# Kernel optimization log

Measured on AMD Instinct MI355X. Metric: run time of the kernel, lower is better.

The kernel has to match this reference:

```python
import jax, jax.numpy as jnp
import numpy as np

N, E = 50000, 800000
IN, HID, OUT = 128, 32, 8


def setup_inputs() -> dict:
    key = jax.random.key(0)
    ks = jax.random.split(key, 20)
    f32 = jnp.float32
    def rn(k, shape, s=0.1):
        return (jax.random.normal(k, shape, dtype=f32) * s)
    return {
        'x': jax.random.normal(ks[0], (N, IN), dtype=f32),
        'edge_index': jax.random.randint(ks[1], (2, E), 0, N, dtype=jnp.int32),
        'edge_attr': jax.random.uniform(ks[2], (E, 1), dtype=f32),
        # layer 1: heads=4, out=HID, concat -> 4*HID channels
        'w1l': rn(ks[3], (IN, 4 * HID)), 'b1l': rn(ks[4], (4 * HID,)),
        'w1r': rn(ks[5], (IN, 4 * HID)), 'b1r': rn(ks[6], (4 * HID,)),
        'w1e': rn(ks[7], (1, 4 * HID)),
        'att1': rn(ks[8], (4, HID)), 'bias1': rn(ks[9], (4 * HID,)),
        # layer 2: heads=2, out=HID, mean over heads -> HID channels
        'w2l': rn(ks[10], (4 * HID, 2 * HID)), 'b2l': rn(ks[11], (2 * HID,)),
        'w2r': rn(ks[12], (4 * HID, 2 * HID)), 'b2r': rn(ks[13], (2 * HID,)),
        'w2e': rn(ks[14], (1, 2 * HID)),
        'att2': rn(ks[15], (2, HID)), 'bias2': rn(ks[16], (HID,)),
        'wc': rn(ks[17], (HID, OUT)), 'bc': rn(ks[18], (OUT,)),
    }


def _add_self_loops(edge_index, edge_attr, n):
    # PyG GATv2Conv adds self-loops; edge feature for loops = mean of edge_attr
    loop = jnp.arange(n, dtype=edge_index.dtype)
    src = jnp.concatenate([edge_index[0], loop])
    dst = jnp.concatenate([edge_index[1], loop])
    mean_attr = jnp.broadcast_to(edge_attr.mean(axis=0), (n, edge_attr.shape[1]))
    ea = jnp.concatenate([edge_attr, mean_attr], axis=0)
    return src, dst, ea


def _gatv2(x, src, dst, eattr, Wl, bl, Wr, br, We, att, bias, heads, out, concat):
    n = x.shape[0]
    xl = (x @ Wl + bl).reshape(n, heads, out)   # source transform (messages)
    xr = (x @ Wr + br).reshape(n, heads, out)   # target transform
    e = (eattr @ We).reshape(-1, heads, out)    # edge embedding
    z = jax.nn.leaky_relu(xl[src] + xr[dst] + e, negative_slope=0.2)  # [Etot,H,D]
    score = jnp.einsum('ehd,hd->eh', z, att)
    # segment softmax over incoming edges of each destination node
    smax = jax.ops.segment_max(score, dst, num_segments=n)
    ex = jnp.exp(score - smax[dst])
    denom = jax.ops.segment_sum(ex, dst, num_segments=n)
    alpha = ex / denom[dst]                     # [Etot,H]
    agg = jax.ops.segment_sum(xl[src] * alpha[..., None], dst, num_segments=n)
    o = agg.reshape(n, heads * out) if concat else agg.mean(axis=1)
    return o + bias


def reference(x, edge_index, edge_attr, w1l, b1l, w1r, b1r, w1e, att1, bias1,
              w2l, b2l, w2r, b2r, w2e, att2, bias2, wc, bc):
    src, dst, ea = _add_self_loops(edge_index, edge_attr, x.shape[0])
    h = _gatv2(x, src, dst, ea, w1l, b1l, w1r, b1r, w1e, att1, bias1, 4, HID, True)
    h = jax.nn.elu(h)
    # dropout p=0.4 is training-only; reference is eval mode (identity)
    h = _gatv2(h, src, dst, ea, w2l, b2l, w2r, b2r, w2e, att2, bias2, 2, HID, False)
    h = jax.nn.elu(h)
    return h @ wc + bc
```

## Files before the change

### kernel.cpp

```cpp
#include <hip/hip_runtime.h>
#include <hip/hip_fp16.h>
#include <math.h>

typedef _Float16 h2_t __attribute__((ext_vector_type(2)));
typedef _Float16 h4_t __attribute__((ext_vector_type(4)));
typedef _Float16 h8_t __attribute__((ext_vector_type(8)));
typedef float f4_t __attribute__((ext_vector_type(4)));
typedef float f8_t __attribute__((ext_vector_type(8)));

#define PRE_BLOCKS 512
#define SB 512
#define NBUK_PAD 800

__device__ inline h8_t load8f_to_h8(const float* p) {
    float4 a = *(const float4*)p;
    float4 b = *(const float4*)(p + 4);
    h8_t r;
    r[0] = (_Float16)a.x; r[1] = (_Float16)a.y; r[2] = (_Float16)a.z; r[3] = (_Float16)a.w;
    r[4] = (_Float16)b.x; r[5] = (_Float16)b.y; r[6] = (_Float16)b.z; r[7] = (_Float16)b.w;
    return r;
}

__device__ inline h4_t load4f_to_h4(const float* p) {
    float4 a = *(const float4*)p;
    h4_t r;
    r[0] = (_Float16)a.x; r[1] = (_Float16)a.y; r[2] = (_Float16)a.z; r[3] = (_Float16)a.w;
    return r;
}

__device__ inline float dot8h(h8_t a, h8_t b, float s) {
    s = __builtin_amdgcn_fdot2(__builtin_shufflevector(a, a, 0, 1),
                               __builtin_shufflevector(b, b, 0, 1), s, false);
    s = __builtin_amdgcn_fdot2(__builtin_shufflevector(a, a, 2, 3),
                               __builtin_shufflevector(b, b, 2, 3), s, false);
    s = __builtin_amdgcn_fdot2(__builtin_shufflevector(a, a, 4, 5),
                               __builtin_shufflevector(b, b, 4, 5), s, false);
    s = __builtin_amdgcn_fdot2(__builtin_shufflevector(a, a, 6, 7),
                               __builtin_shufflevector(b, b, 6, 7), s, false);
    return s;
}

__device__ inline float dot4h(h4_t a, h4_t b, float s) {
    s = __builtin_amdgcn_fdot2(__builtin_shufflevector(a, a, 0, 1),
                               __builtin_shufflevector(b, b, 0, 1), s, false);
    s = __builtin_amdgcn_fdot2(__builtin_shufflevector(a, a, 2, 3),
                               __builtin_shufflevector(b, b, 2, 3), s, false);
    return s;
}

__device__ inline float elu1(float v) { return v > 0.f ? v : __expf(v) - 1.f; }

struct MA {
    const float* x;
    const float* eattr;
    const int* ei;
    const float *w1l, *b1l, *w1r, *b1r, *w1e, *att1, *bias1;
    const float *w2l, *b2l, *w2r, *b2r, *w2e, *att2, *bias2;
    const float *wc, *bc;
    float* out;
    _Float16 *xh, *xl1h, *xr1h, *h1h, *xl2h, *xr2h;
    _Float16 *p1l, *p1r, *p2l, *p2r;
    int *deg, *offb;
    unsigned* parth;
    unsigned *tstart, *tot;
    unsigned* smeanq;
    unsigned long long* tmp;
    unsigned* flags;
    float* part;
    unsigned* edges;
    int N, E, NW, NBK, CE;
    float invE;
};


__device__ inline void phase_packw(const MA& a, int g) {
    const float* W;
    _Float16* P;
    int M, lg;
    if (g < 2048)      { W = a.w1l; P = a.p1l; M = 128; lg = g; }
    else if (g < 4096) { W = a.w1r; P = a.p1r; M = 128; lg = g - 2048; }
    else if (g < 5120) { W = a.w2l; P = a.p2l; M = 64;  lg = g - 4096; }
    else               { W = a.w2r; P = a.p2r; M = 64;  lg = g - 5120; }
    int ln = lg & 63;
    int s = (lg >> 6) & 3;
    int tt = lg >> 8;
    int m = ln & 15, quad = ln >> 4;
    h8_t v;
#pragma unroll
    for (int j = 0; j < 8; ++j)
        v[j] = (_Float16)W[(size_t)(s * 32 + quad * 8 + j) * M + tt * 16 + m];
    *(h8_t*)(P + (size_t)lg * 8) = v;
}

template <int NT>
__device__ inline void phase_mm_tile(const MA& a, const _Float16* X, int rt, int lane,
                                     const _Float16* Pl, const float* bl, _Float16* Yl,
                                     const _Float16* Pr, const float* br, _Float16* Yr) {
    int nrow = lane & 15, quad = lane >> 4;
    int row = rt * 16 + nrow;
    if (row >= a.N) return;
    const _Float16* xp = X + (size_t)row * 128 + quad * 8;
    h8_t bf0 = *(const h8_t*)(xp);
    h8_t bf1 = *(const h8_t*)(xp + 32);
    h8_t bf2 = *(const h8_t*)(xp + 64);
    h8_t bf3 = *(const h8_t*)(xp + 96);
#pragma unroll
    for (int w = 0; w < 2; ++w) {
        const _Float16* P = w ? Pr : Pl;
        const float* bias = w ? br : bl;
        _Float16* Y = w ? Yr : Yl;
#pragma unroll
        for (int t2 = 0; t2 < NT; ++t2) {
            f4_t acc = {0.f, 0.f, 0.f, 0.f};
            const _Float16* pb = P + (size_t)t2 * 2048 + (size_t)lane * 8;
            acc = __builtin_amdgcn_mfma_f32_16x16x32_f16(*(const h8_t*)pb, bf0, acc, 0, 0, 0);
            acc = __builtin_amdgcn_mfma_f32_16x16x32_f16(*(const h8_t*)(pb + 512), bf1, acc, 0, 0, 0);
            acc = __builtin_amdgcn_mfma_f32_16x16x32_f16(*(const h8_t*)(pb + 1024), bf2, acc, 0, 0, 0);
            acc = __builtin_amdgcn_mfma_f32_16x16x32_f16(*(const h8_t*)(pb + 1536), bf3, acc, 0, 0, 0);
            float4 bv = *(const float4*)(bias + t2 * 16 + quad * 4);
            h4_t o;
            o[0] = (_Float16)(acc[0] + bv.x);
            o[1] = (_Float16)(acc[1] + bv.y);
            o[2] = (_Float16)(acc[2] + bv.z);
            o[3] = (_Float16)(acc[3] + bv.w);
            *(h4_t*)(Y + (size_t)row * (NT * 16) + t2 * 16 + quad * 4) = o;
        }
    }
}


__global__ __launch_bounds__(256) void k_pre(MA a) {
    if (blockIdx.x >= PRE_BLOCKS) {
        int g = (blockIdx.x - PRE_BLOCKS) * 256 + threadIdx.x;
        if (g < 6144) phase_packw(a, g);
        return;
    }
    __shared__ unsigned bh[NBUK_PAD];
    __shared__ float sd[4];
    int tx = threadIdx.x;
    for (int j = tx; j < NBUK_PAD; j += 256) bh[j] = 0u;

    int t = blockIdx.x * 256 + tx;
    const int stride = PRE_BLOCKS * 256;
    for (int i = t; i < NBUK_PAD; i += stride) a.flags[i] = 0u;
    int nchunk = (a.N * 128) >> 3;
    for (int i = t; i < nchunk; i += stride) {
        h8_t v = load8f_to_h8(a.x + (size_t)i * 8);
        *(h8_t*)(a.xh + (size_t)i * 8) = v;
    }
    float s = 0.f;
    for (int i = t; i < a.E; i += stride) s += a.eattr[i];
    for (int o = 1; o < 64; o <<= 1) s += __shfl_xor(s, o, 64);
    if ((tx & 63) == 0) sd[tx >> 6] = s;
    __syncthreads();
    if (tx == 0) a.part[blockIdx.x] = sd[0] + sd[1] + sd[2] + sd[3];

    int e0 = blockIdx.x * a.CE, e1 = min(e0 + a.CE, a.E);
    for (int e = e0 + tx; e < e1; e += 256)
        atomicAdd(&bh[((unsigned)a.ei[a.E + e]) >> 6], 1u);
    __syncthreads();
    for (int j = tx; j < NBUK_PAD; j += 256)
        a.parth[(size_t)blockIdx.x * NBUK_PAD + j] = bh[j];
}


__global__ __launch_bounds__(512, 1) void k_colscan(MA a) {
    __shared__ unsigned lds[512];
    __shared__ unsigned sbase;
    __shared__ float sd[8];
    int tx = threadIdx.x;
    int b = blockIdx.x;
    unsigned v = a.parth[(size_t)tx * NBUK_PAD + b];
    lds[tx] = v;
    __syncthreads();
    for (int o = 1; o < 512; o <<= 1) {
        unsigned u = (tx >= o) ? lds[tx - o] : 0u;
        __syncthreads();
        lds[tx] += u;
        __syncthreads();
    }
    unsigned T = lds[511];
    unsigned excl = lds[tx] - v;
    if (tx == 0) {
        unsigned run = 0;
        if (b == 0) {
            atomicExch(&a.flags[0], (2u << 30) | T);
        } else {
            atomicExch(&a.flags[b], (1u << 30) | T);
            int j = b - 1;
            while (true) {
                unsigned f = atomicAdd(&a.flags[j], 0u);
                unsigned st = f >> 30;
                if (st == 0u) continue;
                run += f & 0x3FFFFFFFu;
                if (st == 2u) break;
                --j;
            }
            atomicExch(&a.flags[b], (2u << 30) | (run + T));
        }
        a.tstart[b] = run;
        a.tot[b] = T;
        sbase = run;
    }
    __syncthreads();
    a.parth[(size_t)tx * NBUK_PAD + b] = sbase + excl;

    if (b == 0) {
        float s = a.part[tx];
        for (int o = 1; o < 64; o <<= 1) s += __shfl_xor(s, o, 64);
        if ((tx & 63) == 0) sd[tx >> 6] = s;
        __syncthreads();
        if (tx == 0) {
            float m = 0.f;
#pragma unroll
            for (int k = 0; k < 8; ++k) m += sd[k];
            a.smeanq[0] = (unsigned)__float2int_rn(m * a.invE * 255.f);
        }
    }
}


__global__ __launch_bounds__(256) void k_scatter(MA a) {
    int bid = blockIdx.x;
    if (bid < a.NW) {
        int wid = bid * 4 + (threadIdx.x >> 6);
        int ntile = (a.N + 15) / 16;
        if (wid < ntile)
            phase_mm_tile<8>(a, a.xh, wid, threadIdx.x & 63,
                             a.p1l, a.b1l, a.xl1h, a.p1r, a.b1r, a.xr1h);
        return;
    }
    __shared__ unsigned cur[NBUK_PAD];
    int s = bid - a.NW;
    int tx = threadIdx.x;
    for (int j = tx; j < NBUK_PAD; j += 256)
        cur[j] = a.parth[(size_t)s * NBUK_PAD + j];
    __syncthreads();
    int e0 = s * a.CE, e1 = min(e0 + a.CE, a.E);
    for (int e = e0 + tx; e < e1; e += 256) {
        int d = a.ei[a.E + e];
        unsigned src = (unsigned)a.ei[e];
        unsigned q = (unsigned)__float2int_rn(a.eattr[e] * 255.f);
        unsigned pos = atomicAdd(&cur[d >> 6], 1u);
        a.tmp[pos] = ((unsigned long long)(unsigned)(d & 63) << 32) |
                     (unsigned long long)(src | (q << 24));
    }
}


__global__ __launch_bounds__(256) void k_fine(MA a) {
    __shared__ int hist[64];
    __shared__ unsigned cur[64];
    __shared__ unsigned sm;
    int b = blockIdx.x;
    int tx = threadIdx.x;
    int n0 = b << 6;
    int nn = min(64, a.N - n0);
    unsigned ts = a.tstart[b], T = a.tot[b];
    if (tx < 64) hist[tx] = 0;
    if (tx == 0) sm = a.smeanq[0];
    __syncthreads();
    for (unsigned i = tx; i < T; i += 256) {
        unsigned long long v = a.tmp[ts + i];
        atomicAdd(&hist[(int)((v >> 32) & 63)], 1);
    }
    __syncthreads();
    if (tx < 64) {
        int deg1 = hist[tx] + 1;
        int vsc = deg1;
#pragma unroll
        for (int o = 1; o < 64; o <<= 1) {
            int u = __shfl_up(vsc, o, 64);
            if (tx >= o) vsc += u;
        }
        int off = (int)ts + n0 + (vsc - deg1);
        if (tx < nn) {
            a.offb[n0 + tx] = off;
            a.deg[n0 + tx] = deg1;
            a.edges[off] = (unsigned)(n0 + tx) | (sm << 24);
        }
        cur[tx] = (unsigned)(off + 1);
    }
    __syncthreads();
    for (unsigned i = tx; i < T; i += 256) {
        unsigned long long v = a.tmp[ts + i];
        int loc = (int)((v >> 32) & 63);
        unsigned pos = atomicAdd(&cur[loc], 1u);
        a.edges[pos] = (unsigned)v;
    }
}


__global__ __launch_bounds__(256) void k_node1(MA a) {
    int tid = threadIdx.x;
    int q = tid & 15;
    int node = blockIdx.x * 16 + (tid >> 4);
    if (node >= a.N) return;
    unsigned cb = (unsigned)(q * 16);

    h8_t xrv = *(const h8_t*)((const char*)a.xr1h + ((unsigned)node << 8) + cb);
    h8_t wev = load8f_to_h8(a.w1e + q * 8);
    h8_t atv = load8f_to_h8(a.att1 + q * 8);
    const unsigned* ep = a.edges + a.offb[node];
    int deg1 = a.deg[node];
    int last = deg1 - 1;
    const char* xb = (const char*)a.xl1h;

    float l = 0.f;
    f8_t acc = {0.f, 0.f, 0.f, 0.f, 0.f, 0.f, 0.f, 0.f};
    for (int i = 0; i < deg1; i += 4) {
        unsigned p0 = ep[i];
        unsigned p1 = ep[min(i + 1, last)];
        unsigned p2 = ep[min(i + 2, last)];
        unsigned p3 = ep[min(i + 3, last)];
        h8_t x0 = *(const h8_t*)(xb + (((p0 & 0x00FFFFFFu) << 8) | cb));
        h8_t x1 = *(const h8_t*)(xb + (((p1 & 0x00FFFFFFu) << 8) | cb));
        h8_t x2 = *(const h8_t*)(xb + (((p2 & 0x00FFFFFFu) << 8) | cb));
        h8_t x3 = *(const h8_t*)(xb + (((p3 & 0x00FFFFFFu) << 8) | cb));
        float e0 = (float)(p0 >> 24) * (1.f / 255.f);
        float e1 = (float)(p1 >> 24) * (1.f / 255.f);
        float e2 = (float)(p2 >> 24) * (1.f / 255.f);
        float e3 = (float)(p3 >> 24) * (1.f / 255.f);
        h8_t z0 = x0 + xrv + wev * (_Float16)e0;
        z0 = __builtin_elementwise_max(z0, z0 * (_Float16)0.2f);
        float sc0 = dot8h(z0, atv, 0.f);
        h8_t z1 = x1 + xrv + wev * (_Float16)e1;
        z1 = __builtin_elementwise_max(z1, z1 * (_Float16)0.2f);
        float sc1 = dot8h(z1, atv, 0.f);
        h8_t z2 = x2 + xrv + wev * (_Float16)e2;
        z2 = __builtin_elementwise_max(z2, z2 * (_Float16)0.2f);
        float sc2 = dot8h(z2, atv, 0.f);
        h8_t z3 = x3 + xrv + wev * (_Float16)e3;
        z3 = __builtin_elementwise_max(z3, z3 * (_Float16)0.2f);
        float sc3 = dot8h(z3, atv, 0.f);
        sc0 += __shfl_xor(sc0, 1, 64); sc0 += __shfl_xor(sc0, 2, 64);
        sc1 += __shfl_xor(sc1, 1, 64); sc1 += __shfl_xor(sc1, 2, 64);
        sc2 += __shfl_xor(sc2, 1, 64); sc2 += __shfl_xor(sc2, 2, 64);
        sc3 += __shfl_xor(sc3, 1, 64); sc3 += __shfl_xor(sc3, 2, 64);
        float pA = __expf(fminf(sc0, 60.f));
        float pB = (i + 1 < deg1) ? __expf(fminf(sc1, 60.f)) : 0.f;
        float pC = (i + 2 < deg1) ? __expf(fminf(sc2, 60.f)) : 0.f;
        float pD = (i + 3 < deg1) ? __expf(fminf(sc3, 60.f)) : 0.f;
        l += (pA + pB) + (pC + pD);
#pragma unroll
        for (int k = 0; k < 8; ++k)
            acc[k] = fmaf(pA, (float)x0[k],
                     fmaf(pB, (float)x1[k],
                     fmaf(pC, (float)x2[k], fmaf(pD, (float)x3[k], acc[k]))));
    }
    float inv = 1.f / l;
    float4 b0 = *(const float4*)(a.bias1 + q * 8);
    float4 b1 = *(const float4*)(a.bias1 + q * 8 + 4);
    float bb[8] = {b0.x, b0.y, b0.z, b0.w, b1.x, b1.y, b1.z, b1.w};
    h8_t o;
#pragma unroll
    for (int k = 0; k < 8; ++k) o[k] = (_Float16)elu1(fmaf(acc[k], inv, bb[k]));
    *(h8_t*)((char*)a.h1h + ((unsigned)node << 8) + cb) = o;
}


__global__ __launch_bounds__(256) void k_mm4(MA a) {
    int wid = blockIdx.x * 4 + (threadIdx.x >> 6);
    int ntile = (a.N + 15) / 16;
    if (wid >= ntile) return;
    phase_mm_tile<4>(a, a.h1h, wid, threadIdx.x & 63,
                     a.p2l, a.b2l, a.xl2h, a.p2r, a.b2r, a.xr2h);
}


__global__ __launch_bounds__(256) void k_node2(MA a) {
    __shared__ float h2s[16][33];
    int tid = threadIdx.x;
    int lane = tid & 63;
    int wib = tid >> 6;
    int sub = lane >> 4;
    int r = lane & 15;
    int nloc = wib * 4 + sub;
    int node = blockIdx.x * 16 + nloc;
    int c0 = r * 4;

    if (node < a.N) {
        h4_t xrv = *(const h4_t*)(a.xr2h + (size_t)node * 64 + c0);
        h4_t wev = load4f_to_h4(a.w2e + c0);
        h4_t atv = load4f_to_h4(a.att2 + c0);
        const unsigned* ep = a.edges + a.offb[node];
        int deg1 = a.deg[node];
        int last = deg1 - 1;
        const char* xb = (const char*)a.xl2h;
        unsigned cb = (unsigned)(c0 * 2);
        float l = 0.f;
        float acc[4] = {0.f, 0.f, 0.f, 0.f};
        for (int i = 0; i < deg1; i += 4) {
            unsigned p[4];
            h4_t xv[4];
#pragma unroll
            for (int j = 0; j < 4; ++j) p[j] = ep[min(i + j, last)];
#pragma unroll
            for (int j = 0; j < 4; ++j)
                xv[j] = *(const h4_t*)(xb + (((p[j] & 0x00FFFFFFu) << 7) | cb));
#pragma unroll
            for (int j = 0; j < 4; ++j) {
                float ea = (float)(p[j] >> 24) * (1.f / 255.f);
                h4_t z = xv[j] + xrv + wev * (_Float16)ea;
                z = __builtin_elementwise_max(z, z * (_Float16)0.2f);
                float sc = dot4h(z, atv, 0.f);
                sc += __shfl_xor(sc, 1, 64);
                sc += __shfl_xor(sc, 2, 64);
                sc += __shfl_xor(sc, 4, 64);
                float pp = (i + j < deg1) ? __expf(fminf(sc, 60.f)) : 0.f;
                l += pp;
#pragma unroll
                for (int k = 0; k < 4; ++k) acc[k] = fmaf(pp, (float)xv[j][k], acc[k]);
            }
        }
        float inv = 1.f / l;
#pragma unroll
        for (int k = 0; k < 4; ++k) {
            float norm = acc[k] * inv;
            float other = __shfl_xor(norm, 8, 64);
            float v = 0.5f * (norm + other);
            if (r < 8) h2s[nloc][c0 + k] = elu1(v + a.bias2[c0 + k]);
        }
    }
    __syncthreads();
    if (tid < 128) {
        int n = tid >> 3, j = tid & 7;
        int gnode = blockIdx.x * 16 + n;
        if (gnode < a.N) {
            float acc = a.bc[j];
#pragma unroll 8
            for (int d = 0; d < 32; ++d) acc = fmaf(h2s[n][d], a.wc[d * 8 + j], acc);
            a.out[(size_t)gnode * 8 + j] = acc;
        }
    }
}


extern "C" void kernel_launch(void* const* d_in, const int* in_sizes, int n_in,
                              void* d_out, int out_size, void* d_ws, size_t ws_size,
                              hipStream_t stream) {
    const int N = in_sizes[0] / 128;
    const int E = in_sizes[2];
    const int tot = E + N;

    char* ws = (char*)d_ws;
    size_t o = 0;
    auto alloc = [&](size_t bytes) -> void* {
        void* p = ws + o;
        o += (bytes + 255) & ~(size_t)255;
        return p;
    };
    MA a;
    a.x     = (const float*)d_in[0];
    a.ei    = (const int*)d_in[1];
    a.eattr = (const float*)d_in[2];
    a.w1l = (const float*)d_in[3];  a.b1l = (const float*)d_in[4];
    a.w1r = (const float*)d_in[5];  a.b1r = (const float*)d_in[6];
    a.w1e = (const float*)d_in[7];  a.att1 = (const float*)d_in[8];
    a.bias1 = (const float*)d_in[9];
    a.w2l = (const float*)d_in[10]; a.b2l = (const float*)d_in[11];
    a.w2r = (const float*)d_in[12]; a.b2r = (const float*)d_in[13];
    a.w2e = (const float*)d_in[14]; a.att2 = (const float*)d_in[15];
    a.bias2 = (const float*)d_in[16];
    a.wc = (const float*)d_in[17];  a.bc = (const float*)d_in[18];
    a.out = (float*)d_out;

    a.xh   = (_Float16*)alloc((size_t)N * 128 * 2);
    a.xl1h = (_Float16*)alloc((size_t)N * 128 * 2);
    a.xr1h = (_Float16*)alloc((size_t)N * 128 * 2);
    a.h1h  = (_Float16*)alloc((size_t)N * 128 * 2);
    a.xl2h = (_Float16*)alloc((size_t)N * 64 * 2);
    a.xr2h = (_Float16*)alloc((size_t)N * 64 * 2);
    a.p1l  = (_Float16*)alloc(128 * 128 * 2);
    a.p1r  = (_Float16*)alloc(128 * 128 * 2);
    a.p2l  = (_Float16*)alloc(128 * 64 * 2);
    a.p2r  = (_Float16*)alloc(128 * 64 * 2);
    a.deg  = (int*)alloc((size_t)N * 4);
    a.offb = (int*)alloc((size_t)N * 4);
    a.parth  = (unsigned*)alloc((size_t)SB * NBUK_PAD * 4);
    a.tstart = (unsigned*)alloc(NBUK_PAD * 4);
    a.tot    = (unsigned*)alloc(NBUK_PAD * 4);
    a.smeanq = (unsigned*)alloc(256);
    a.flags  = (unsigned*)alloc(1024 * 4);
    a.part   = (float*)alloc(PRE_BLOCKS * 4);
    a.tmp    = (unsigned long long*)alloc((size_t)E * 8);
    a.edges  = (unsigned*)alloc((size_t)tot * 4);
    a.N = N;
    a.E = E;
    a.NW = (N + 63) / 64;
    a.NBK = (N + 63) >> 6;
    a.CE = (E + SB - 1) / SB;
    a.invE = 1.0f / (float)E;

    k_pre<<<PRE_BLOCKS + 24, 256, 0, stream>>>(a);
    k_colscan<<<a.NBK, 512, 0, stream>>>(a);
    k_scatter<<<a.NW + SB, 256, 0, stream>>>(a);
    k_fine<<<a.NBK, 256, 0, stream>>>(a);
    k_node1<<<(N + 15) / 16, 256, 0, stream>>>(a);
    k_mm4<<<(N + 63) / 64, 256, 0, stream>>>(a);
    k_node2<<<(N + 15) / 16, 256, 0, stream>>>(a);
}
```

Baseline: 256.6 us.

## Double-buffer edge gathers in node kernels and pack sort temp to 32-bit

The gather loops in both GATv2 node kernels now use register double buffering. The next group of four source rows is loaded before the current group is computed, so memory latency overlaps the score and softmax math. The intermediate bucket-sort array shrinks from 64-bit to 32-bit entries by packing a 16-bit source index, the 8-bit quantized edge attribute and the 6-bit local destination, which halves its scatter and read traffic. The packing assumes node indices fit in 16 bits, and the doubled live registers may reduce occupancy.

```diff
diff --git a/kernel.cpp b/kernel.cpp
--- a/kernel.cpp
+++ b/kernel.cpp
@@ -64,7 +64,7 @@
     unsigned* parth;
     unsigned *tstart, *tot;
     unsigned* smeanq;
-    unsigned long long* tmp;
+    unsigned* tmp;
     unsigned* flags;
     float* part;
     unsigned* edges;
@@ -242,8 +242,7 @@
         unsigned src = (unsigned)a.ei[e];
         unsigned q = (unsigned)__float2int_rn(a.eattr[e] * 255.f);
         unsigned pos = atomicAdd(&cur[d >> 6], 1u);
-        a.tmp[pos] = ((unsigned long long)(unsigned)(d & 63) << 32) |
-                     (unsigned long long)(src | (q << 24));
+        a.tmp[pos] = src | (q << 16) | ((unsigned)(d & 63) << 24);
     }
 }
 
@@ -261,8 +260,8 @@
     if (tx == 0) sm = a.smeanq[0];
     __syncthreads();
     for (unsigned i = tx; i < T; i += 256) {
-        unsigned long long v = a.tmp[ts + i];
-        atomicAdd(&hist[(int)((v >> 32) & 63)], 1);
+        unsigned v = a.tmp[ts + i];
+        atomicAdd(&hist[(int)(v >> 24)], 1);
     }
     __syncthreads();
     if (tx < 64) {
@@ -283,10 +282,10 @@
     }
     __syncthreads();
     for (unsigned i = tx; i < T; i += 256) {
-        unsigned long long v = a.tmp[ts + i];
-        int loc = (int)((v >> 32) & 63);
+        unsigned v = a.tmp[ts + i];
+        int loc = (int)(v >> 24);
         unsigned pos = atomicAdd(&cur[loc], 1u);
-        a.edges[pos] = (unsigned)v;
+        a.edges[pos] = (v & 0xFFFFu) | (((v >> 16) & 0xFFu) << 24);
     }
 }
 
@@ -308,15 +307,20 @@
 
     float l = 0.f;
     f8_t acc = {0.f, 0.f, 0.f, 0.f, 0.f, 0.f, 0.f, 0.f};
-    for (int i = 0; i < deg1; i += 4) {
-        unsigned p0 = ep[i];
-        unsigned p1 = ep[min(i + 1, last)];
-        unsigned p2 = ep[min(i + 2, last)];
-        unsigned p3 = ep[min(i + 3, last)];
-        h8_t x0 = *(const h8_t*)(xb + (((p0 & 0x00FFFFFFu) << 8) | cb));
-        h8_t x1 = *(const h8_t*)(xb + (((p1 & 0x00FFFFFFu) << 8) | cb));
-        h8_t x2 = *(const h8_t*)(xb + (((p2 & 0x00FFFFFFu) << 8) | cb));
-        h8_t x3 = *(const h8_t*)(xb + (((p3 & 0x00FFFFFFu) << 8) | cb));
+
+    auto GA = [&](unsigned p) -> h8_t {
+        return *(const h8_t*)(xb + (((p & 0x00FFFFFFu) << 8) | cb));
+    };
+    auto LOADG = [&](int i, unsigned& p0, unsigned& p1, unsigned& p2, unsigned& p3,
+                     h8_t& x0, h8_t& x1, h8_t& x2, h8_t& x3) {
+        p0 = ep[i];
+        p1 = ep[min(i + 1, last)];
+        p2 = ep[min(i + 2, last)];
+        p3 = ep[min(i + 3, last)];
+        x0 = GA(p0); x1 = GA(p1); x2 = GA(p2); x3 = GA(p3);
+    };
+    auto COMPG = [&](int i, unsigned p0, unsigned p1, unsigned p2, unsigned p3,
+                     h8_t x0, h8_t x1, h8_t x2, h8_t x3) {
         float e0 = (float)(p0 >> 24) * (1.f / 255.f);
         float e1 = (float)(p1 >> 24) * (1.f / 255.f);
         float e2 = (float)(p2 >> 24) * (1.f / 255.f);
@@ -347,7 +351,18 @@
             acc[k] = fmaf(pA, (float)x0[k],
                      fmaf(pB, (float)x1[k],
                      fmaf(pC, (float)x2[k], fmaf(pD, (float)x3[k], acc[k]))));
-    }
+    };
+
+    unsigned pa0, pa1, pa2, pa3, pb0, pb1, pb2, pb3;
+    h8_t xa0, xa1, xa2, xa3, xb0, xb1, xb2, xb3;
+    LOADG(0, pa0, pa1, pa2, pa3, xa0, xa1, xa2, xa3);
+    for (int i = 0; i < deg1; i += 8) {
+        if (i + 4 < deg1) LOADG(i + 4, pb0, pb1, pb2, pb3, xb0, xb1, xb2, xb3);
+        COMPG(i, pa0, pa1, pa2, pa3, xa0, xa1, xa2, xa3);
+        if (i + 8 < deg1) LOADG(i + 8, pa0, pa1, pa2, pa3, xa0, xa1, xa2, xa3);
+        if (i + 4 < deg1) COMPG(i + 4, pb0, pb1, pb2, pb3, xb0, xb1, xb2, xb3);
+    }
+
     float inv = 1.f / l;
     float4 b0 = *(const float4*)(a.bias1 + q * 8);
     float4 b1 = *(const float4*)(a.bias1 + q * 8 + 4);
@@ -390,29 +405,46 @@
         unsigned cb = (unsigned)(c0 * 2);
         float l = 0.f;
         float acc[4] = {0.f, 0.f, 0.f, 0.f};
-        for (int i = 0; i < deg1; i += 4) {
-            unsigned p[4];
-            h4_t xv[4];
-#pragma unroll
-            for (int j = 0; j < 4; ++j) p[j] = ep[min(i + j, last)];
-#pragma unroll
-            for (int j = 0; j < 4; ++j)
-                xv[j] = *(const h4_t*)(xb + (((p[j] & 0x00FFFFFFu) << 7) | cb));
-#pragma unroll
-            for (int j = 0; j < 4; ++j) {
-                float ea = (float)(p[j] >> 24) * (1.f / 255.f);
-                h4_t z = xv[j] + xrv + wev * (_Float16)ea;
-                z = __builtin_elementwise_max(z, z * (_Float16)0.2f);
-                float sc = dot4h(z, atv, 0.f);
-                sc += __shfl_xor(sc, 1, 64);
-                sc += __shfl_xor(sc, 2, 64);
-                sc += __shfl_xor(sc, 4, 64);
-                float pp = (i + j < deg1) ? __expf(fminf(sc, 60.f)) : 0.f;
-                l += pp;
-#pragma unroll
-                for (int k = 0; k < 4; ++k) acc[k] = fmaf(pp, (float)xv[j][k], acc[k]);
+
+        auto GA = [&](unsigned p) -> h4_t {
+            return *(const h4_t*)(xb + (((p & 0x00FFFFFFu) << 7) | cb));
+        };
+        auto LOADG = [&](int i, unsigned& p0, unsigned& p1, unsigned& p2, unsigned& p3,
+                         h4_t& x0, h4_t& x1, h4_t& x2, h4_t& x3) {
+            p0 = ep[i];
+            p1 = ep[min(i + 1, last)];
+            p2 = ep[min(i + 2, last)];
+            p3 = ep[min(i + 3, last)];
+            x0 = GA(p0); x1 = GA(p1); x2 = GA(p2); x3 = GA(p3);
+        };
+        auto CEDGE = [&](int idx, unsigned p, h4_t xv) {
+            float ea = (float)(p >> 24) * (1.f / 255.f);
+            h4_t z = xv + xrv + wev * (_Float16)ea;
+            z = __builtin_elementwise_max(z, z * (_Float16)0.2f);
+            float sc = dot4h(z, atv, 0.f);
+            sc += __shfl_xor(sc, 1, 64);
+            sc += __shfl_xor(sc, 2, 64);
+            sc += __shfl_xor(sc, 4, 64);
+            float pp = (idx < deg1) ? __expf(fminf(sc, 60.f)) : 0.f;
+            l += pp;
+#pragma unroll
+            for (int k = 0; k < 4; ++k) acc[k] = fmaf(pp, (float)xv[k], acc[k]);
+        };
+
+        unsigned pa0, pa1, pa2, pa3, pb0, pb1, pb2, pb3;
+        h4_t xa0, xa1, xa2, xa3, xb0, xb1, xb2, xb3;
+        LOADG(0, pa0, pa1, pa2, pa3, xa0, xa1, xa2, xa3);
+        for (int i = 0; i < deg1; i += 8) {
+            if (i + 4 < deg1) LOADG(i + 4, pb0, pb1, pb2, pb3, xb0, xb1, xb2, xb3);
+            CEDGE(i, pa0, xa0); CEDGE(i + 1, pa1, xa1);
+            CEDGE(i + 2, pa2, xa2); CEDGE(i + 3, pa3, xa3);
+            if (i + 8 < deg1) LOADG(i + 8, pa0, pa1, pa2, pa3, xa0, xa1, xa2, xa3);
+            if (i + 4 < deg1) {
+                CEDGE(i + 4, pb0, xb0); CEDGE(i + 5, pb1, xb1);
+                CEDGE(i + 6, pb2, xb2); CEDGE(i + 7, pb3, xb3);
             }
         }
+
         float inv = 1.f / l;
 #pragma unroll
         for (int k = 0; k < 4; ++k) {
@@ -483,7 +515,7 @@
     a.smeanq = (unsigned*)alloc(256);
     a.flags  = (unsigned*)alloc(1024 * 4);
     a.part   = (float*)alloc(PRE_BLOCKS * 4);
-    a.tmp    = (unsigned long long*)alloc((size_t)E * 8);
+    a.tmp    = (unsigned*)alloc((size_t)E * 4);
     a.edges  = (unsigned*)alloc((size_t)tot * 4);
     a.N = N;
     a.E = E;
```

Result: slower. 265.1 us (+3.3%).
